# Kernel tuning notes

Hardware: AMD Instinct MI355X
Metric: run time of the kernel (lower is better)

The kernel has to match this reference:

```python
import jax, jax.numpy as jnp
import numpy as np
from jax import lax

B, T, H, W, C = 2, 32, 65, 65, 32
KS = 15   # kernel_size
F = 32    # conv features


def setup_inputs() -> dict:
    key = jax.random.key(0)
    ks = jax.random.split(key, 12)
    d = {}
    d["input_seq"] = jax.random.normal(ks[0], (B, T, H, W, C), jnp.float32)
    d["conv_w"] = jax.random.normal(ks[1], (3, 3, C, F), jnp.float32) / np.sqrt(3 * 3 * C).astype(np.float32)
    d["conv_b"] = jnp.zeros((F,), jnp.float32)
    for i, nm in enumerate(["alpha", "delta", "mu", "gamma"]):
        d[f"w_{nm}"] = jax.random.normal(ks[2 + i], (F, C), jnp.float32) / np.sqrt(F).astype(np.float32)
        d[f"b_{nm}"] = jnp.zeros((C,), jnp.float32)
    # nn.initializers.normal() -> stddev 0.01
    d["k_exc"] = jax.random.normal(ks[10], (KS, KS, C), jnp.float32) * 0.01
    d["k_inh"] = jax.random.normal(ks[11], (KS, KS, C), jnp.float32) * 0.01
    return d


def _kernel_spec(k, Hh, Ww):
    # zero-pad the (KS,KS,C) kernel to (H,W,C), then rfft2 over spatial axes
    ph, pw = (Hh - KS) // 2, (Ww - KS) // 2
    kp = jnp.pad(k, ((ph, ph), (pw, pw), (0, 0)))
    return jnp.fft.rfft2(kp, axes=(0, 1))  # (H, W//2+1, C) complex64


def reference(input_seq, conv_w, conv_b, w_alpha, b_alpha, w_delta, b_delta,
              w_mu, b_mu, w_gamma, b_gamma, k_exc, k_inh):
    Bb, Tt, Hh, Ww, Cc = input_seq.shape
    # context conv: flax Conv flattens leading (B,T) into batch; SAME, stride 2
    x = input_seq.reshape(Bb * Tt, Hh, Ww, Cc)
    stats = lax.conv_general_dilated(x, conv_w, (2, 2), 'SAME',
                                     dimension_numbers=('NHWC', 'HWIO', 'NHWC')) + conv_b
    stats = jax.nn.gelu(stats)  # flax nn.gelu (approximate)
    Hp, Wp = stats.shape[1], stats.shape[2]
    stats = stats.reshape(Bb, Tt, Hp, Wp, F)
    ctx = jnp.mean(stats, axis=(1, 2))                 # (B, Wp, F); Wp == W//2+1 for odd W
    alpha = jax.nn.sigmoid(ctx @ w_alpha + b_alpha)    # (B, Wp, C)
    delta = jax.nn.sigmoid(ctx @ w_delta + b_delta)
    mu = jax.nn.softplus(ctx @ w_mu + b_mu)
    gamma = jax.nn.softplus(ctx @ w_gamma + b_gamma)

    K_E = _kernel_spec(k_exc, Hh, Ww)  # (H, Wr, C)
    K_I = _kernel_spec(k_inh, Hh, Ww)
    Wr = Ww // 2 + 1
    decay = jnp.asarray(0.9, jnp.complex64)

    bc = lambda v: jnp.broadcast_to(v[:, None, :, :].astype(jnp.complex64), (Bb, Hh, Wr, Cc))
    A_xx = decay * bc(alpha)
    A_yy = decay * bc(delta)
    A_xy = -K_I[None] * bc(mu)
    A_yx = K_E[None] * bc(gamma)
    row0 = jnp.stack([A_xx, A_xy], axis=-1)
    row1 = jnp.stack([A_yx, A_yy], axis=-1)
    K_hat = jnp.stack([row0, row1], axis=-2)           # (B, H, Wr, C, 2, 2)

    U_hat = jnp.fft.rfft2(input_seq, axes=(2, 3))      # (B, T, H, Wr, C) complex64
    U_vec = jnp.stack([U_hat, jnp.zeros_like(U_hat)], axis=-1)  # (B,T,H,Wr,C,2)
    A_t = jnp.broadcast_to(K_hat[:, None], (Bb, Tt, Hh, Wr, Cc, 2, 2))

    # associative op for linear SSM: state_t = A_t @ state_{t-1} + u_t
    # (log/exp of the original cancel: exp(log A)=A, exp(State_log)=State)
    def combine(l, r):
        A1, b1 = l
        A2, b2 = r
        A = jnp.einsum('...ij,...jk->...ik', A2, A1)
        b = jnp.einsum('...ij,...j->...i', A2, b1) + b2
        return A, b

    _, S = lax.associative_scan(combine, (A_t, U_vec), axis=1)
    Y = S[..., 1]                                      # inhibitory component
    return jnp.fft.irfft2(Y, axes=(2, 3))              # (B, T, H, 2*(Wr-1), C) float32
```

## Files before the change

kernel.cpp:

```cpp
#include <hip/hip_runtime.h>
#include <cmath>

#define NB 2
#define NT 32
#define NH 65
#define NW 65
#define NC 32
#define NF 32
#define NKS 15
#define NHP 33
#define NWP 33
#define NWR 33
#define NWOUT 64
#define PI_F 3.14159265358979323846f

__global__ __launch_bounds__(256) void setup_kernel(
    const float* __restrict__ w, float* __restrict__ wT,
    float2* __restrict__ twr, float2* __restrict__ twb, float2* __restrict__ twi)
{
    int blk = blockIdx.x;
    if (blk < 10) {
        int tid = blk * 256 + threadIdx.x;
        if (tid < NH * 36) {
            int q = tid / 36, wr = tid % 36;
            float2 v = make_float2(0.f, 0.f);
            if (wr < NWR) {
                int p = (q * wr) % NH;
                float a = -2.f * PI_F * (float)p / (float)NH;
                v = make_float2(cosf(a), sinf(a));
            }
            twr[tid] = v;
        }
        if (tid < NH * 14) {
            int h = tid / 14, b = tid % 14;
            float2 v = make_float2(0.f, 0.f);
            if (b < 13) {
                int p = (h * b) % NH;
                float a = 2.f * PI_F * (float)p / (float)NH;
                v = make_float2(cosf(a), sinf(a));
            }
            twb[tid] = v;
        }
        if (tid < 31 * 64) {
            int q = tid / 64 + 1, ow = tid % 64;
            int p = (q * ow) & 63;
            float a = 2.f * PI_F * (float)p / (float)NWOUT;
            twi[tid] = make_float2(cosf(a), sinf(a));
        }
    } else {
        int tid = (blk - 10) * 256 + threadIdx.x;
        if (tid < 9 * NC * NF) {
            int dd = tid / 1024;
            int rem = tid % 1024;
            int q = rem / 128;
            int r2 = rem % 128;
            int f = r2 / 4;
            int cj = r2 % 4;
            wT[tid] = w[((size_t)dd * NC + 4 * q + cj) * NF + f];
        }
    }
}

#define DOT4(acc, a, wv) \
    acc = fmaf((a).x, (wv).x, fmaf((a).y, (wv).y, fmaf((a).z, (wv).z, fmaf((a).w, (wv).w, acc))))

__global__ __launch_bounds__(256) void conv_stats_kernel(
    const float* __restrict__ x, const float* __restrict__ wT,
    const float* __restrict__ bias, float* __restrict__ partial)
{
    __shared__ float4 rows4[3 * 68 * 8];
    __shared__ float4 wsh4[9 * 8 * 32];
    int blk = blockIdx.x;
    int b = blk / (NT * NHP);
    int r = blk % (NT * NHP);
    int t = r / NHP;
    int i = r % NHP;
    int tid = threadIdx.x;

    const float4* wsrc = (const float4*)wT;
    for (int idx = tid; idx < 9 * 8 * 32; idx += 256) wsh4[idx] = wsrc[idx];

    const float4* xb4 = (const float4*)(x + ((size_t)(b * NT + t) * NH) * (NW * NC));
    for (int idx = tid; idx < 3 * 544; idx += 256) {
        int di = idx / 544;
        int k = idx % 544;
        int row = 2 * i - 1 + di;
        float4 v = make_float4(0.f, 0.f, 0.f, 0.f);
        if (row >= 0 && row < NH && k >= 8 && k < 528)
            v = xb4[row * 520 + (k - 8)];
        rows4[idx] = v;
    }
    __syncthreads();

    int f = tid & 31;
    int jg = tid >> 5;
    float bv = bias[f];
    float acc0 = bv, acc1 = bv, acc2 = bv, acc3 = bv;

    for (int q = 0; q < 8; ++q) {
        #pragma unroll
        for (int di = 0; di < 3; ++di) {
            const float4* rp = &rows4[(di * 68 + 8 * jg) * 8 + q];
            float4 a0 = rp[0],  a1 = rp[8],  a2 = rp[16], a3 = rp[24], a4 = rp[32];
            float4 a5 = rp[40], a6 = rp[48], a7 = rp[56], a8 = rp[64];
            const float4* wp = &wsh4[(di * 3) * 256 + q * 32 + f];
            float4 w0 = wp[0], w1 = wp[256], w2 = wp[512];
            DOT4(acc0, a0, w0); DOT4(acc0, a1, w1); DOT4(acc0, a2, w2);
            DOT4(acc1, a2, w0); DOT4(acc1, a3, w1); DOT4(acc1, a4, w2);
            DOT4(acc2, a4, w0); DOT4(acc2, a5, w1); DOT4(acc2, a6, w2);
            DOT4(acc3, a6, w0); DOT4(acc3, a7, w1); DOT4(acc3, a8, w2);
        }
    }

    float acc4 = bv;
    if (jg == 0) {
        for (int q = 0; q < 8; ++q) {
            #pragma unroll
            for (int di = 0; di < 3; ++di) {
                const float4* rp = &rows4[(di * 68 + 64) * 8 + q];
                float4 a0 = rp[0], a1 = rp[8], a2 = rp[16];
                const float4* wp = &wsh4[(di * 3) * 256 + q * 32 + f];
                float4 w0 = wp[0], w1 = wp[256], w2 = wp[512];
                DOT4(acc4, a0, w0); DOT4(acc4, a1, w1); DOT4(acc4, a2, w2);
            }
        }
    }

    float* pout = partial + ((size_t)b * (NT * NHP) + (t * NHP + i)) * (NWP * NF);
    #define GELU(v) (0.5f * (v) * (1.f + tanhf(0.7978845608028654f * ((v) + 0.044715f * (v) * (v) * (v)))))
    pout[(4 * jg + 0) * NF + f] = GELU(acc0);
    pout[(4 * jg + 1) * NF + f] = GELU(acc1);
    pout[(4 * jg + 2) * NF + f] = GELU(acc2);
    pout[(4 * jg + 3) * NF + f] = GELU(acc3);
    if (jg == 0) pout[32 * NF + f] = GELU(acc4);
    #undef GELU
}

__global__ __launch_bounds__(256) void ctx_reduce1_kernel(
    const float* __restrict__ partial, float* __restrict__ red2)
{
    __shared__ float red[4][64];
    int blk = blockIdx.x;
    int b = blk / 136;
    int rem = blk % 136;
    int chunk = rem / 8;
    int ts = rem % 8;
    int lane = threadIdx.x & 63;
    int tig = threadIdx.x >> 6;
    int jf = chunk * 64 + lane;
    float s0 = 0.f, s1 = 0.f, s2 = 0.f;
    if (jf < NWP * NF) {
        const float* p = partial + (size_t)b * (NT * NHP) * (NWP * NF)
                       + (size_t)(ts * 132 + tig * 33) * (NWP * NF) + jf;
        #pragma unroll 3
        for (int s = 0; s < 33; s += 3) {
            s0 += p[(size_t)s * (NWP * NF)];
            s1 += p[(size_t)(s + 1) * (NWP * NF)];
            s2 += p[(size_t)(s + 2) * (NWP * NF)];
        }
    }
    red[tig][lane] = s0 + s1 + s2;
    __syncthreads();
    if (threadIdx.x < 64) {
        float tot = red[0][threadIdx.x] + red[1][threadIdx.x] +
                    red[2][threadIdx.x] + red[3][threadIdx.x];
        red2[((b * 17 + chunk) * 8 + ts) * 64 + threadIdx.x] = tot;
    }
}

__global__ __launch_bounds__(256) void ctx_reduce2_kernel(
    const float* __restrict__ red2, float* __restrict__ ctx)
{
    __shared__ float red[4][64];
    int b = blockIdx.x / 17, chunk = blockIdx.x % 17;
    int lane = threadIdx.x & 63, tg = threadIdx.x >> 6;
    const float* r2 = red2 + ((size_t)(b * 17 + chunk) * 8) * 64;
    float v = r2[(2 * tg) * 64 + lane] + r2[(2 * tg + 1) * 64 + lane];
    red[tg][lane] = v;
    __syncthreads();
    if (threadIdx.x < 64) {
        int jf = chunk * 64 + threadIdx.x;
        if (jf < NWP * NF) {
            float tot = red[0][threadIdx.x] + red[1][threadIdx.x] +
                        red[2][threadIdx.x] + red[3][threadIdx.x];
            ctx[b * (NWP * NF) + jf] = tot * (1.f / (NT * NHP));
        }
    }
}

__global__ __launch_bounds__(256) void gate_kernel(
    const float* __restrict__ ctx,
    const float* __restrict__ wA, const float* __restrict__ bA,
    const float* __restrict__ wD, const float* __restrict__ bD,
    const float* __restrict__ wM, const float* __restrict__ bM,
    const float* __restrict__ wG, const float* __restrict__ bG,
    float* __restrict__ alpha, float* __restrict__ delta,
    float* __restrict__ mu, float* __restrict__ gamma)
{
    int idx = blockIdx.x * 256 + threadIdx.x;
    if (idx >= NB * NWP * NC) return;
    int c = idx % NC;
    int bw = idx / NC;
    float sA = bA[c], sD = bD[c], sM = bM[c], sG = bG[c];
    #pragma unroll
    for (int f = 0; f < NF; ++f) {
        float v = ctx[bw * NF + f];
        sA = fmaf(v, wA[f * NC + c], sA);
        sD = fmaf(v, wD[f * NC + c], sD);
        sM = fmaf(v, wM[f * NC + c], sM);
        sG = fmaf(v, wG[f * NC + c], sG);
    }
    alpha[idx] = 1.f / (1.f + expf(-sA));
    delta[idx] = 1.f / (1.f + expf(-sD));
    mu[idx]    = fmaxf(sM, 0.f) + log1pf(expf(-fabsf(sM)));
    gamma[idx] = fmaxf(sG, 0.f) + log1pf(expf(-fabsf(sG)));
}

__global__ __launch_bounds__(256) void spec_kernel(
    const float* __restrict__ kexc, const float* __restrict__ kinh,
    float2* __restrict__ KE, float2* __restrict__ KI)
{
    __shared__ float2 tw[NH];
    int tid = threadIdx.x;
    if (tid < NH) {
        float a = -2.f * PI_F * (float)tid / (float)NH;
        tw[tid] = make_float2(cosf(a), sinf(a));
    }
    __syncthreads();
    int idx = blockIdx.x * 256 + tid;
    if (idx >= NH * NWR * NC) return;
    int c = idx % NC;
    int rem = idx / NC;
    int wr = rem % NWR;
    int h = rem / NWR;
    float ker = 0, kei = 0, kir = 0, kii = 0;
    int prow = (25 * (h + wr)) % NH;
    for (int i = 0; i < NKS; ++i) {
        int p = prow;
        for (int j = 0; j < NKS; ++j) {
            float2 e = tw[p];
            float ve = kexc[(i * NKS + j) * NC + c];
            float vi = kinh[(i * NKS + j) * NC + c];
            ker = fmaf(ve, e.x, ker); kei = fmaf(ve, e.y, kei);
            kir = fmaf(vi, e.x, kir); kii = fmaf(vi, e.y, kii);
            p += wr; if (p >= NH) p -= NH;
        }
        prow += h; if (prow >= NH) prow -= NH;
    }
    KE[idx] = make_float2(ker, kei);
    KI[idx] = make_float2(kir, kii);
}

__global__ __launch_bounds__(256) void dft_rows_kernel(
    const float* __restrict__ x, const float2* __restrict__ twr_g,
    float2* __restrict__ U1)
{
    __shared__ __align__(16) float row[4][NW * NC];
    __shared__ __align__(16) float2 twt[NH * 36];
    int tid = threadIdx.x;
    int blk = blockIdx.x;
    int grp = blk % 17;
    int bt = blk / 17;
    int hbase = grp * 4;
    int nrows = NH - hbase; if (nrows > 4) nrows = 4;

    const float* xp = x + ((size_t)bt * NH + hbase) * (NW * NC);
    for (int idx = tid; idx < nrows * NW * NC; idx += 256) ((float*)row)[idx] = xp[idx];
    for (int idx = tid; idx < NH * 36; idx += 256) twt[idx] = twr_g[idx];
    __syncthreads();

    int c = tid & 31;
    int jg = tid >> 5;
    float2 acc[4][4];
    #pragma unroll
    for (int r = 0; r < 4; ++r)
        #pragma unroll
        for (int k = 0; k < 4; ++k) acc[r][k] = make_float2(0.f, 0.f);

    const float2* tp = twt + 4 * jg;
    #pragma unroll 5
    for (int q = 0; q < NW; ++q) {
        float4 e01 = *(const float4*)&tp[q * 36];
        float4 e23 = *(const float4*)&tp[q * 36 + 2];
        #pragma unroll
        for (int r = 0; r < 4; ++r) {
            float v = row[r][q * NC + c];
            acc[r][0].x = fmaf(v, e01.x, acc[r][0].x); acc[r][0].y = fmaf(v, e01.y, acc[r][0].y);
            acc[r][1].x = fmaf(v, e01.z, acc[r][1].x); acc[r][1].y = fmaf(v, e01.w, acc[r][1].y);
            acc[r][2].x = fmaf(v, e23.x, acc[r][2].x); acc[r][2].y = fmaf(v, e23.y, acc[r][2].y);
            acc[r][3].x = fmaf(v, e23.z, acc[r][3].x); acc[r][3].y = fmaf(v, e23.w, acc[r][3].y);
        }
    }
    #pragma unroll
    for (int r = 0; r < 4; ++r) {
        if (r < nrows) {
            float2* up = U1 + ((size_t)bt * NH + hbase + r) * (NWR * NC);
            up[(4 * jg + 0) * NC + c] = acc[r][0];
            up[(4 * jg + 1) * NC + c] = acc[r][1];
            up[(4 * jg + 2) * NC + c] = acc[r][2];
            up[(4 * jg + 3) * NC + c] = acc[r][3];
        }
    }
    if (jg == 0) {
        float2 a32[4];
        #pragma unroll
        for (int r = 0; r < 4; ++r) a32[r] = make_float2(0.f, 0.f);
        #pragma unroll 5
        for (int q = 0; q < NW; ++q) {
            float2 e = twt[q * 36 + 32];
            #pragma unroll
            for (int r = 0; r < 4; ++r) {
                float v = row[r][q * NC + c];
                a32[r].x = fmaf(v, e.x, a32[r].x);
                a32[r].y = fmaf(v, e.y, a32[r].y);
            }
        }
        #pragma unroll
        for (int r = 0; r < 4; ++r)
            if (r < nrows)
                U1[((size_t)bt * NH + hbase + r) * (NWR * NC) + 32 * NC + c] = a32[r];
    }
}

template <int SIGN>
__device__ inline void compute5(const float2 v[5], float2* outp) {
    const float C5[5] = {1.f, 0.30901699437494742f, -0.80901699437494745f,
                         -0.80901699437494745f, 0.30901699437494742f};
    const float S5[5] = {0.f, 0.95105651629515357f, 0.58778525229247314f,
                         -0.58778525229247314f, -0.95105651629515357f};
    #pragma unroll
    for (int r = 0; r < 5; ++r) {
        float re = 0.f, im = 0.f;
        #pragma unroll
        for (int a = 0; a < 5; ++a) {
            const int m = (r * a) % 5;
            const float ex = C5[m];
            const float ey = (float)SIGN * S5[m];
            re = fmaf(v[a].x, ex, fmaf(-v[a].y, ey, re));
            im = fmaf(v[a].x, ey, fmaf(v[a].y, ex, im));
        }
        outp[r * NC] = make_float2(re, im);
    }
}

template <int SIGN, bool SCALE>
__global__ __launch_bounds__(256) void dft_cols_kernel(
    const float2* __restrict__ in, float2* __restrict__ out,
    const float2* __restrict__ twb_g)
{
    __shared__ __align__(16) float2 col[NH * NC];
    __shared__ __align__(16) float2 twb[NH * 14];
    int tid = threadIdx.x;
    int blk = blockIdx.x;
    int wr = blk % NWR;
    int bt = blk / NWR;
    const float2* ip = in + ((size_t)bt * NH) * (NWR * NC) + wr * NC;
    for (int idx = tid; idx < NH * NC; idx += 256) {
        int p = idx >> 5, c = idx & 31;
        col[idx] = ip[(size_t)p * (NWR * NC) + c];
    }
    for (int idx = tid; idx < NH * 14; idx += 256) twb[idx] = twb_g[idx];
    __syncthreads();

    float2 va0[5], va1[5];
    int bq0 = tid >> 5, c0 = tid & 31;
    int q1 = tid + 256;
    int bq1 = q1 >> 5, c1 = q1 & 31;
    #pragma unroll
    for (int a = 0; a < 5; ++a) {
        va0[a] = col[(13 * a + bq0) * NC + c0];
        if (q1 < 416) va1[a] = col[(13 * a + bq1) * NC + c1];
    }
    __syncthreads();
    compute5<SIGN>(va0, &col[(bq0 * 5) * NC + c0]);
    if (q1 < 416) compute5<SIGN>(va1, &col[(bq1 * 5) * NC + c1]);
    __syncthreads();

    const float S = (float)SIGN;
    int c = tid & 31;
    int h0 = tid >> 5;
    const float s = SCALE ? (1.f / (float)NH) : 1.f;
    float2* op = out + ((size_t)bt * NH) * (NWR * NC) + wr * NC;
    float2 acc[8];
    #pragma unroll
    for (int k = 0; k < 8; ++k) {
        int h = h0 + 8 * k;
        int r = h % 5;
        const float2* Ap = col + r * NC + c;
        const float2* tp = twb + h * 14;
        float re = 0.f, im = 0.f;
        #pragma unroll
        for (int p = 0; p < 6; ++p) {
            float4 tq = *(const float4*)&tp[2 * p];
            float2 v0 = Ap[(2 * p) * 5 * NC];
            float2 v1 = Ap[(2 * p + 1) * 5 * NC];
            re = fmaf(v0.x, tq.x, fmaf(-S * v0.y, tq.y, re));
            im = fmaf(S * v0.x, tq.y, fmaf(v0.y, tq.x, im));
            re = fmaf(v1.x, tq.z, fmaf(-S * v1.y, tq.w, re));
            im = fmaf(S * v1.x, tq.w, fmaf(v1.y, tq.z, im));
        }
        {
            float2 t12 = tp[12];
            float2 v = Ap[12 * 5 * NC];
            re = fmaf(v.x, t12.x, fmaf(-S * v.y, t12.y, re));
            im = fmaf(S * v.x, t12.y, fmaf(v.y, t12.x, im));
        }
        acc[k] = make_float2(re * s, im * s);
    }
    #pragma unroll
    for (int k = 0; k < 8; ++k) {
        int h = h0 + 8 * k;
        op[(size_t)h * (NWR * NC) + c] = acc[k];
    }
    if (h0 == 0) {
        const float2* Ap = col + 4 * NC + c;
        const float2* tp = twb + 64 * 14;
        float re = 0.f, im = 0.f;
        #pragma unroll
        for (int p = 0; p < 6; ++p) {
            float4 tq = *(const float4*)&tp[2 * p];
            float2 v0 = Ap[(2 * p) * 5 * NC];
            float2 v1 = Ap[(2 * p + 1) * 5 * NC];
            re = fmaf(v0.x, tq.x, fmaf(-S * v0.y, tq.y, re));
            im = fmaf(S * v0.x, tq.y, fmaf(v0.y, tq.x, im));
            re = fmaf(v1.x, tq.z, fmaf(-S * v1.y, tq.w, re));
            im = fmaf(S * v1.x, tq.w, fmaf(v1.y, tq.z, im));
        }
        {
            float2 t12 = tp[12];
            float2 v = Ap[12 * 5 * NC];
            re = fmaf(v.x, t12.x, fmaf(-S * v.y, t12.y, re));
            im = fmaf(S * v.x, t12.y, fmaf(v.y, t12.x, im));
        }
        op[(size_t)64 * (NWR * NC) + c] = make_float2(re * s, im * s);
    }
}

__global__ __launch_bounds__(256) void scan_kernel(
    float2* __restrict__ buf, const float2* __restrict__ KE,
    const float2* __restrict__ KI, const float* __restrict__ alpha,
    const float* __restrict__ delta, const float* __restrict__ mu,
    const float* __restrict__ gamma)
{
    int idx = blockIdx.x * 256 + threadIdx.x;
    if (idx >= NB * NH * NWR * NC) return;
    int c = idx % NC;
    int rem = idx / NC;
    int wr = rem % NWR;
    int rem2 = rem / NWR;
    int h = rem2 % NH;
    int b = rem2 / NH;

    int gi = (b * NWP + wr) * NC + c;
    float axx = 0.9f * alpha[gi];
    float ayy = 0.9f * delta[gi];
    float m = mu[gi], g = gamma[gi];
    float2 ki = KI[(h * NWR + wr) * NC + c];
    float2 ke = KE[(h * NWR + wr) * NC + c];
    float2 axy = make_float2(-ki.x * m, -ki.y * m);
    float2 ayx = make_float2(ke.x * g, ke.y * g);

    float2 xs = make_float2(0.f, 0.f), ys = make_float2(0.f, 0.f);
    size_t base = ((size_t)b * NT) * NH * NWR * NC + (size_t)h * (NWR * NC) + wr * NC + c;
    const size_t stride = (size_t)NH * NWR * NC;
    for (int t = 0; t < NT; ++t) {
        float2 U = buf[base + (size_t)t * stride];
        float2 nx, ny;
        nx.x = fmaf(axx, xs.x, fmaf(axy.x, ys.x, fmaf(-axy.y, ys.y, U.x)));
        nx.y = fmaf(axx, xs.y, fmaf(axy.x, ys.y, fmaf(axy.y, ys.x, U.y)));
        ny.x = fmaf(ayx.x, xs.x, fmaf(-ayx.y, xs.y, ayy * ys.x));
        ny.y = fmaf(ayx.x, xs.y, fmaf(ayx.y, xs.x, ayy * ys.y));
        xs = nx; ys = ny;
        buf[base + (size_t)t * stride] = ys;
    }
}

__global__ __launch_bounds__(256) void irfft_w_kernel(
    const float2* __restrict__ Z, const float2* __restrict__ twi_g,
    float* __restrict__ out)
{
    __shared__ __align__(16) float2 z[4][NWR * NC];
    __shared__ __align__(16) float2 twi[31 * 64];
    int tid = threadIdx.x;
    int blk = blockIdx.x;
    int grp = blk % 17;
    int bt = blk / 17;
    int hbase = grp * 4;
    int nrows = NH - hbase; if (nrows > 4) nrows = 4;

    const float2* zp = Z + ((size_t)bt * NH + hbase) * (NWR * NC);
    for (int idx = tid; idx < nrows * NWR * NC; idx += 256) ((float2*)z)[idx] = zp[idx];
    for (int idx = tid; idx < 31 * 64; idx += 256) twi[idx] = twi_g[idx];
    __syncthreads();

    int c = tid & 31;
    int g = tid >> 5;
    float acc[4][8];
    #pragma unroll
    for (int r = 0; r < 4; ++r) {
        float z0 = z[r][c].x;
        float zn = z[r][32 * NC + c].x;
        #pragma unroll
        for (int m = 0; m < 8; ++m) acc[r][m] = z0 + ((m & 1) ? -zn : zn);
    }
    const float2* tp = twi + 8 * g;
    for (int q = 1; q < 32; ++q) {
        const float4* tq = (const float4*)&tp[(q - 1) * 64];
        float4 e0 = tq[0], e1 = tq[1], e2 = tq[2], e3 = tq[3];
        #pragma unroll
        for (int r = 0; r < 4; ++r) {
            float2 v = z[r][q * NC + c];
            float vx = 2.f * v.x, vy = 2.f * v.y;
            acc[r][0] = fmaf(vx, e0.x, fmaf(-vy, e0.y, acc[r][0]));
            acc[r][1] = fmaf(vx, e0.z, fmaf(-vy, e0.w, acc[r][1]));
            acc[r][2] = fmaf(vx, e1.x, fmaf(-vy, e1.y, acc[r][2]));
            acc[r][3] = fmaf(vx, e1.z, fmaf(-vy, e1.w, acc[r][3]));
            acc[r][4] = fmaf(vx, e2.x, fmaf(-vy, e2.y, acc[r][4]));
            acc[r][5] = fmaf(vx, e2.z, fmaf(-vy, e2.w, acc[r][5]));
            acc[r][6] = fmaf(vx, e3.x, fmaf(-vy, e3.y, acc[r][6]));
            acc[r][7] = fmaf(vx, e3.z, fmaf(-vy, e3.w, acc[r][7]));
        }
    }
    #pragma unroll
    for (int r = 0; r < 4; ++r) {
        if (r < nrows) {
            float* op = out + ((size_t)bt * NH + hbase + r) * (NWOUT * NC);
            #pragma unroll
            for (int m = 0; m < 8; ++m)
                op[(8 * g + m) * NC + c] = acc[r][m] * (1.f / (float)NWOUT);
        }
    }
}

extern "C" void kernel_launch(void* const* d_in, const int* in_sizes, int n_in,
                              void* d_out, int out_size, void* d_ws, size_t ws_size,
                              hipStream_t stream)
{
    const float* x     = (const float*)d_in[0];
    const float* convw = (const float*)d_in[1];
    const float* convb = (const float*)d_in[2];
    const float* wA = (const float*)d_in[3];
    const float* bA = (const float*)d_in[4];
    const float* wD = (const float*)d_in[5];
    const float* bD = (const float*)d_in[6];
    const float* wM = (const float*)d_in[7];
    const float* bM = (const float*)d_in[8];
    const float* wG = (const float*)d_in[9];
    const float* bG = (const float*)d_in[10];
    const float* kexc = (const float*)d_in[11];
    const float* kinh = (const float*)d_in[12];

    const size_t NBIG = (size_t)NB * NT * NH * NWR * NC;
    char* ws = (char*)d_ws;
    float2* bufA    = (float2*)ws;  ws += NBIG * sizeof(float2);
    float2* KE      = (float2*)ws;  ws += (size_t)NH * NWR * NC * sizeof(float2);
    float2* KI      = (float2*)ws;  ws += (size_t)NH * NWR * NC * sizeof(float2);
    float*  partial = (float*)ws;   ws += (size_t)NB * (NT * NHP) * (NWP * NF) * sizeof(float);
    float*  ctx     = (float*)ws;   ws += (size_t)NB * NWP * NF * sizeof(float);
    float*  red2    = (float*)ws;   ws += (size_t)NB * 17 * 8 * 64 * sizeof(float);
    float*  alpha   = (float*)ws;   ws += (size_t)NB * NWP * NC * sizeof(float);
    float*  delta   = (float*)ws;   ws += (size_t)NB * NWP * NC * sizeof(float);
    float*  mu      = (float*)ws;   ws += (size_t)NB * NWP * NC * sizeof(float);
    float*  gamma   = (float*)ws;   ws += (size_t)NB * NWP * NC * sizeof(float);
    float2* TWR     = (float2*)ws;  ws += (size_t)NH * 36 * sizeof(float2);
    float2* TWB     = (float2*)ws;  ws += (size_t)NH * 14 * sizeof(float2);
    float2* TWI     = (float2*)ws;  ws += (size_t)31 * 64 * sizeof(float2);
    float*  wT      = (float*)ws;   ws += (size_t)9 * NC * NF * sizeof(float);

    setup_kernel<<<46, 256, 0, stream>>>(convw, wT, TWR, TWB, TWI);

    conv_stats_kernel<<<NB * NT * NHP, 256, 0, stream>>>(x, wT, convb, partial);
    ctx_reduce1_kernel<<<NB * 136, 256, 0, stream>>>(partial, red2);
    ctx_reduce2_kernel<<<NB * 17, 256, 0, stream>>>(red2, ctx);
    gate_kernel<<<(NB * NWP * NC + 255) / 256, 256, 0, stream>>>(
        ctx, wA, bA, wD, bD, wM, bM, wG, bG, alpha, delta, mu, gamma);

    spec_kernel<<<(NH * NWR * NC + 255) / 256, 256, 0, stream>>>(kexc, kinh, KE, KI);

    dft_rows_kernel<<<NB * NT * 17, 256, 0, stream>>>(x, TWR, bufA);
    dft_cols_kernel<-1, false><<<NB * NT * NWR, 256, 0, stream>>>(bufA, bufA, TWB);

    scan_kernel<<<(NB * NH * NWR * NC + 255) / 256, 256, 0, stream>>>(
        bufA, KE, KI, alpha, delta, mu, gamma);

    dft_cols_kernel<+1, true><<<NB * NT * NWR, 256, 0, stream>>>(bufA, bufA, TWB);
    irfft_w_kernel<<<NB * NT * 17, 256, 0, stream>>>(bufA, TWI, (float*)d_out);
}
```

Baseline: 204.5 us.

## Run context conv on MFMA with split-bf16 (hi/lo) emulation of fp32

Replaces the scalar-FMA stride-2 3x3 context convolution with a matrix-core version using bf16 16x16x32 MFMA. Activations and weights are split into high and low bf16 parts, and three MFMA products (lo*hi, hi*lo, hi*hi) approximate fp32 accuracy. The aim is to cut the ALU cost of the conv stage. In exchange it adds conversion work when staging into LDS, triples the MFMA count, and loses a little precision compared with full fp32.

```diff
diff --git a/kernel.cpp b/kernel.cpp
--- a/kernel.cpp
+++ b/kernel.cpp
@@ -14,8 +14,24 @@
 #define NWOUT 64
 #define PI_F 3.14159265358979323846f
 
+using bf16x8 = __attribute__((ext_vector_type(8))) __bf16;
+using f32x4  = __attribute__((ext_vector_type(4))) float;
+using s16x4  = __attribute__((ext_vector_type(4))) short;
+
+__device__ inline unsigned short f2bf(float v) {
+    unsigned u = __float_as_uint(v);
+    u = u + 0x7FFF + ((u >> 16) & 1);
+    return (unsigned short)(u >> 16);
+}
+__device__ inline float bf2f(unsigned short h) {
+    return __uint_as_float((unsigned)h << 16);
+}
+
+union FragU { s16x4 h[2]; bf16x8 v; };
+
 __global__ __launch_bounds__(256) void setup_kernel(
-    const float* __restrict__ w, float* __restrict__ wT,
+    const float* __restrict__ w, unsigned short* __restrict__ wBh,
+    unsigned short* __restrict__ wBl,
     float2* __restrict__ twr, float2* __restrict__ twb, float2* __restrict__ twi)
 {
     int blk = blockIdx.x;
@@ -49,90 +65,112 @@
         }
     } else {
         int tid = (blk - 10) * 256 + threadIdx.x;
-        if (tid < 9 * NC * NF) {
+        if (tid < 9 * NF * NC) {
             int dd = tid / 1024;
-            int rem = tid % 1024;
-            int q = rem / 128;
-            int r2 = rem % 128;
-            int f = r2 / 4;
-            int cj = r2 % 4;
-            wT[tid] = w[((size_t)dd * NC + 4 * q + cj) * NF + f];
-        }
-    }
-}
-
-#define DOT4(acc, a, wv) \
-    acc = fmaf((a).x, (wv).x, fmaf((a).y, (wv).y, fmaf((a).z, (wv).z, fmaf((a).w, (wv).w, acc))))
-
-__global__ __launch_bounds__(256) void conv_stats_kernel(
-    const float* __restrict__ x, const float* __restrict__ wT,
-    const float* __restrict__ bias, float* __restrict__ partial)
-{
-    __shared__ float4 rows4[3 * 68 * 8];
-    __shared__ float4 wsh4[9 * 8 * 32];
+            int f = (tid / 32) % 32;
+            int c = tid % 32;
+            float v = w[((size_t)dd * NC + c) * NF + f];
+            unsigned short h = f2bf(v);
+            wBh[tid] = h;
+            wBl[tid] = f2bf(v - bf2f(h));
+        }
+    }
+}
+
+__global__ __launch_bounds__(256) void conv_mfma_kernel(
+    const float* __restrict__ x, const unsigned short* __restrict__ wBh,
+    const unsigned short* __restrict__ wBl, const float* __restrict__ bias,
+    float* __restrict__ partial)
+{
+    __shared__ unsigned short aH[3 * 68 * 36];
+    __shared__ unsigned short aL[3 * 68 * 36];
     int blk = blockIdx.x;
-    int b = blk / (NT * NHP);
-    int r = blk % (NT * NHP);
-    int t = r / NHP;
-    int i = r % NHP;
+    int i = blk % NHP;
+    int bt = blk / NHP;
     int tid = threadIdx.x;
-
-    const float4* wsrc = (const float4*)wT;
-    for (int idx = tid; idx < 9 * 8 * 32; idx += 256) wsh4[idx] = wsrc[idx];
-
-    const float4* xb4 = (const float4*)(x + ((size_t)(b * NT + t) * NH) * (NW * NC));
-    for (int idx = tid; idx < 3 * 544; idx += 256) {
-        int di = idx / 544;
-        int k = idx % 544;
-        int row = 2 * i - 1 + di;
+    int l = tid & 63;
+    int w = tid >> 6;
+
+    int nt = w & 1;
+    int fcol = nt * 16 + (l & 15);
+    int c0 = (l >> 4) * 8;
+    bf16x8 bh[9], bl[9];
+    #pragma unroll
+    for (int dd = 0; dd < 9; ++dd) {
+        bh[dd] = *(const bf16x8*)(wBh + dd * 1024 + fcol * 32 + c0);
+        bl[dd] = *(const bf16x8*)(wBl + dd * 1024 + fcol * 32 + c0);
+    }
+
+    const float* xb = x + (size_t)bt * (NH * NW * NC);
+    for (int q = tid; q < 3 * 68 * 8; q += 256) {
+        int r = q / 544;
+        int k = q % 544;
+        int pcol = k >> 3;
+        int c4 = (k & 7) * 4;
+        int gr = 2 * i - 1 + r;
+        int gcol = pcol - 1;
         float4 v = make_float4(0.f, 0.f, 0.f, 0.f);
-        if (row >= 0 && row < NH && k >= 8 && k < 528)
-            v = xb4[row * 520 + (k - 8)];
-        rows4[idx] = v;
-    }
-    __syncthreads();
-
-    int f = tid & 31;
-    int jg = tid >> 5;
-    float bv = bias[f];
-    float acc0 = bv, acc1 = bv, acc2 = bv, acc3 = bv;
-
-    for (int q = 0; q < 8; ++q) {
-        #pragma unroll
-        for (int di = 0; di < 3; ++di) {
-            const float4* rp = &rows4[(di * 68 + 8 * jg) * 8 + q];
-            float4 a0 = rp[0],  a1 = rp[8],  a2 = rp[16], a3 = rp[24], a4 = rp[32];
-            float4 a5 = rp[40], a6 = rp[48], a7 = rp[56], a8 = rp[64];
-            const float4* wp = &wsh4[(di * 3) * 256 + q * 32 + f];
-            float4 w0 = wp[0], w1 = wp[256], w2 = wp[512];
-            DOT4(acc0, a0, w0); DOT4(acc0, a1, w1); DOT4(acc0, a2, w2);
-            DOT4(acc1, a2, w0); DOT4(acc1, a3, w1); DOT4(acc1, a4, w2);
-            DOT4(acc2, a4, w0); DOT4(acc2, a5, w1); DOT4(acc2, a6, w2);
-            DOT4(acc3, a6, w0); DOT4(acc3, a7, w1); DOT4(acc3, a8, w2);
-        }
-    }
-
-    float acc4 = bv;
-    if (jg == 0) {
-        for (int q = 0; q < 8; ++q) {
-            #pragma unroll
-            for (int di = 0; di < 3; ++di) {
-                const float4* rp = &rows4[(di * 68 + 64) * 8 + q];
-                float4 a0 = rp[0], a1 = rp[8], a2 = rp[16];
-                const float4* wp = &wsh4[(di * 3) * 256 + q * 32 + f];
-                float4 w0 = wp[0], w1 = wp[256], w2 = wp[512];
-                DOT4(acc4, a0, w0); DOT4(acc4, a1, w1); DOT4(acc4, a2, w2);
-            }
-        }
-    }
-
-    float* pout = partial + ((size_t)b * (NT * NHP) + (t * NHP + i)) * (NWP * NF);
+        if (gr >= 0 && gr < NH && gcol >= 0 && gcol < NW)
+            v = *(const float4*)(xb + ((size_t)gr * NW + gcol) * NC + c4);
+        int base = (r * 68 + pcol) * 36 + c4;
+        unsigned short h0 = f2bf(v.x), h1 = f2bf(v.y), h2 = f2bf(v.z), h3 = f2bf(v.w);
+        s16x4 th = {(short)h0, (short)h1, (short)h2, (short)h3};
+        *(s16x4*)(aH + base) = th;
+        s16x4 tl = {(short)f2bf(v.x - bf2f(h0)), (short)f2bf(v.y - bf2f(h1)),
+                    (short)f2bf(v.z - bf2f(h2)), (short)f2bf(v.w - bf2f(h3))};
+        *(s16x4*)(aL + base) = tl;
+    }
+    __syncthreads();
+
+    float bv = bias[fcol];
+    f32x4 acc0 = {bv, bv, bv, bv};
+    f32x4 acc1 = {bv, bv, bv, bv};
+    const int mtA = (w >> 1) ? 1 : 0;
+    const bool hasB = (w >> 1) == 0;
+    int m15 = l & 15;
+
+    #pragma unroll
+    for (int dd = 0; dd < 9; ++dd) {
+        const int di = dd / 3, dj = dd % 3;
+        {
+            int pcol = 2 * (mtA * 16 + m15) + dj;
+            int off = (di * 68 + pcol) * 36 + c0;
+            FragU ah, al;
+            ah.h[0] = *(const s16x4*)(aH + off);
+            ah.h[1] = *(const s16x4*)(aH + off + 4);
+            al.h[0] = *(const s16x4*)(aL + off);
+            al.h[1] = *(const s16x4*)(aL + off + 4);
+            acc0 = __builtin_amdgcn_mfma_f32_16x16x32_bf16(al.v, bh[dd], acc0, 0, 0, 0);
+            acc0 = __builtin_amdgcn_mfma_f32_16x16x32_bf16(ah.v, bl[dd], acc0, 0, 0, 0);
+            acc0 = __builtin_amdgcn_mfma_f32_16x16x32_bf16(ah.v, bh[dd], acc0, 0, 0, 0);
+        }
+        if (hasB) {
+            int pcol = 2 * (32 + m15) + dj;
+            if (pcol > 67) pcol = 67;
+            int off = (di * 68 + pcol) * 36 + c0;
+            FragU ah, al;
+            ah.h[0] = *(const s16x4*)(aH + off);
+            ah.h[1] = *(const s16x4*)(aH + off + 4);
+            al.h[0] = *(const s16x4*)(aL + off);
+            al.h[1] = *(const s16x4*)(aL + off + 4);
+            acc1 = __builtin_amdgcn_mfma_f32_16x16x32_bf16(al.v, bh[dd], acc1, 0, 0, 0);
+            acc1 = __builtin_amdgcn_mfma_f32_16x16x32_bf16(ah.v, bl[dd], acc1, 0, 0, 0);
+            acc1 = __builtin_amdgcn_mfma_f32_16x16x32_bf16(ah.v, bh[dd], acc1, 0, 0, 0);
+        }
+    }
+
+    float* pout = partial + (size_t)blk * (NWP * NF);
+    int g4 = (l >> 4) * 4;
     #define GELU(v) (0.5f * (v) * (1.f + tanhf(0.7978845608028654f * ((v) + 0.044715f * (v) * (v) * (v)))))
-    pout[(4 * jg + 0) * NF + f] = GELU(acc0);
-    pout[(4 * jg + 1) * NF + f] = GELU(acc1);
-    pout[(4 * jg + 2) * NF + f] = GELU(acc2);
-    pout[(4 * jg + 3) * NF + f] = GELU(acc3);
-    if (jg == 0) pout[32 * NF + f] = GELU(acc4);
+    #pragma unroll
+    for (int r = 0; r < 4; ++r) {
+        float v = acc0[r];
+        pout[(mtA * 16 + g4 + r) * NF + fcol] = GELU(v);
+    }
+    if (hasB && g4 == 0) {
+        float v = acc1[0];
+        pout[32 * NF + fcol] = GELU(v);
+    }
     #undef GELU
 }
 
@@ -565,11 +603,12 @@
     float2* TWR     = (float2*)ws;  ws += (size_t)NH * 36 * sizeof(float2);
     float2* TWB     = (float2*)ws;  ws += (size_t)NH * 14 * sizeof(float2);
     float2* TWI     = (float2*)ws;  ws += (size_t)31 * 64 * sizeof(float2);
-    float*  wT      = (float*)ws;   ws += (size_t)9 * NC * NF * sizeof(float);
-
-    setup_kernel<<<46, 256, 0, stream>>>(convw, wT, TWR, TWB, TWI);
-
-    conv_stats_kernel<<<NB * NT * NHP, 256, 0, stream>>>(x, wT, convb, partial);
+    unsigned short* wBh = (unsigned short*)ws; ws += (size_t)9 * NC * NF * sizeof(unsigned short);
+    unsigned short* wBl = (unsigned short*)ws; ws += (size_t)9 * NC * NF * sizeof(unsigned short);
+
+    setup_kernel<<<46, 256, 0, stream>>>(convw, wBh, wBl, TWR, TWB, TWI);
+
+    conv_mfma_kernel<<<NB * NT * NHP, 256, 0, stream>>>(x, wBh, wBl, convb, partial);
     ctx_reduce1_kernel<<<NB * 136, 256, 0, stream>>>(partial, red2);
     ctx_reduce2_kernel<<<NB * 17, 256, 0, stream>>>(red2, ctx);
     gate_kernel<<<(NB * NWP * NC + 255) / 256, 256, 0, stream>>>(
```

New measurement: 175.6 us. 14.1% less time.
